# Performance work log

Measured on AMD Instinct MI355X. Metric: run time of the kernel, lower is better.

Reference implementation:

```python
import jax, jax.numpy as jnp
import numpy as np

SCALE = 0.2  # scale init arg, clipped to [0,1]


def _relative_corners(rank):
    # [2**rank, rank] matrix of +-1 corner coordinates
    return jnp.array([[float(int(c)) * 2.0 - 1.0 for c in format(i, '0%db' % rank)]
                      for i in range(2 ** rank)], dtype=jnp.float32)


def _affine_from_noise(random_u):
    # random_u: [B, 2**r, r] uniform(0,1) -> random_scale uniform(1-SCALE, 1)
    B, n, r = random_u.shape
    out_c = _relative_corners(r)                                  # [2^r, r]
    random_scale = (1.0 - SCALE) + SCALE * random_u
    src = out_c[None] * random_scale                              # [B, 2^r, r]
    ones_col = jnp.ones((B, n, 1), jnp.float32)
    A = jnp.broadcast_to(
        jnp.concatenate([out_c, jnp.ones((n, 1), jnp.float32)], -1)[None],
        (B, n, r + 1))                                            # output corners (homog.)
    Bmat = jnp.concatenate([src, ones_col], -1)                   # source corners (homog.)
    # least-squares solve A X = B  (matrix_solve_ls): X = (A^T A)^{-1} A^T B
    AtA = jnp.einsum('bni,bnj->bij', A, A)
    AtB = jnp.einsum('bni,bnj->bij', A, Bmat)
    X = jnp.linalg.solve(AtA, AtB)                                # [B, r+1, r+1]
    return jnp.transpose(X, (0, 2, 1))                            # transform, [B, r+1, r+1]


def _make_grid(transform, spatial_shape):
    # AffineGridWarper: output voxel coords normalized to [-1,1], affine-mapped,
    # then converted to source pixel coordinates [0, size-1].
    r = len(spatial_shape)
    axes = [jnp.linspace(-1.0, 1.0, s) for s in spatial_shape]
    mesh = jnp.stack(jnp.meshgrid(*axes, indexing='ij'), -1)      # [D,H,W,r]
    mesh_h = jnp.concatenate(
        [mesh, jnp.ones(tuple(spatial_shape) + (1,), jnp.float32)], -1)
    coords = jnp.einsum('dhwj,bij->bdhwi', mesh_h, transform[:, :r, :])  # [B,D,H,W,r]
    sizes = jnp.array(spatial_shape, jnp.float32)
    return (coords + 1.0) * (sizes - 1.0) * 0.5                   # pixel coords


def _resample_linear_zero(img, coords):
    # trilinear interpolation with zero boundary: out-of-range corners contribute 0
    # img: [B,D,H,W,C], coords: [B,D,H,W,3] (pixel coordinates)
    B = img.shape[0]
    sp = jnp.array(img.shape[1:4], jnp.int32)
    f = jnp.floor(coords)
    frac = coords - f                                             # [B,D,H,W,3]
    i0 = f.astype(jnp.int32)
    bidx = jnp.arange(B)[:, None, None, None]
    out = jnp.zeros(img.shape, img.dtype)
    for corner in range(8):  # fixed structural loop over 2^3 interpolation corners
        off = jnp.array([(corner >> 2) & 1, (corner >> 1) & 1, corner & 1], jnp.int32)
        idx = i0 + off
        valid = jnp.all((idx >= 0) & (idx < sp), axis=-1)         # [B,D,H,W]
        ci = jnp.clip(idx, 0, sp - 1)
        vals = img[bidx, ci[..., 0], ci[..., 1], ci[..., 2]]      # [B,D,H,W,C]
        w = jnp.prod(jnp.where(off == 1, frac, 1.0 - frac), axis=-1)
        w = w * valid.astype(img.dtype)
        out = out + vals * w[..., None]
    return out


def setup_inputs() -> dict:
    key = jax.random.key(0)
    k1, k2 = jax.random.split(key)
    input_tensor = jax.random.normal(k1, (8, 128, 128, 128, 1), dtype=jnp.float32)
    random_u = jax.random.uniform(k2, (8, 8, 3), dtype=jnp.float32)
    return {"input_tensor": input_tensor, "random_u": random_u}


def reference(input_tensor, random_u):
    transform = _affine_from_noise(random_u)                      # [B,4,4]
    grid = _make_grid(transform, input_tensor.shape[1:4])         # [B,D,H,W,3]
    return _resample_linear_zero(input_tensor, grid)
```

## Files before the change

### kernel.cpp

```cpp
#include <hip/hip_runtime.h>

#define NB   8
#define NS   128
#define VOX  (NS*NS*NS)

#define SD    13
#define SH    13
#define ROW_W 40
#define RST   (SH*ROW_W)
#define SLAB  (SD*RST)

typedef __attribute__((address_space(1))) const void gconst_t;
typedef __attribute__((address_space(3))) void lds_t;

__global__ __launch_bounds__(256) void warp_resample_kernel(
        const float* __restrict__ img, const float* __restrict__ u,
        float* __restrict__ out) {
    __shared__ __align__(16) float slab[SLAB];

    const int tid = threadIdx.x;
    const int bi   = blockIdx.x;
    const int b    =  bi & 7;
    const int idx  =  bi >> 3;
    const int wblk =  idx & 3;
    const int hblk = (idx >> 2) & 15;
    const int dblk =  idx >> 6;

    const float* ub = u + b * 24;
    float T[3][4];
#pragma unroll
    for (int i = 0; i < 3; ++i) {
        float v[8];
#pragma unroll
        for (int n = 0; n < 8; ++n) {
            const float sg = (n & (4 >> i)) ? 1.f : -1.f;
            v[n] = fmaf(sg * 0.025f, ub[n * 3 + i], sg * 0.1f);
        }
        const float a0 = v[0] + v[1], a1 = v[2] + v[3];
        const float a2 = v[4] + v[5], a3 = v[6] + v[7];
        const float d0 = v[1] - v[0], d1 = v[3] - v[2];
        const float d2 = v[5] - v[4], d3 = v[7] - v[6];
        const float A01 = a0 + a1, A23 = a2 + a3;
        T[i][0] = A23 - A01;
        T[i][1] = (a1 - a0) + (a3 - a2);
        T[i][2] = (d0 + d1) + (d2 + d3);
        T[i][3] = A01 + A23;
    }
    const float t00 = T[0][0], t01 = T[0][1], t02 = T[0][2], t03 = T[0][3];
    const float t10 = T[1][0], t11 = T[1][1], t12 = T[1][2], t13 = T[1][3];
    const float t20 = T[2][0], t21 = T[2][1], t22 = T[2][2], t23 = T[2][3];

    const int d0i = dblk << 3, h0i = hblk << 3, w0i = wblk << 5;
    const float inv = 2.0f / 127.0f;
    const float x0 = -1.f + d0i * inv, y0 = -1.f + h0i * inv, z0 = -1.f + w0i * inv;
    const float P0 = (t00 * x0 + t01 * y0 + t02 * z0 + t03 + 1.f) * 63.5f;
    const float P1 = (t10 * x0 + t11 * y0 + t12 * z0 + t13 + 1.f) * 63.5f;
    const float P2 = (t20 * x0 + t21 * y0 + t22 * z0 + t23 + 1.f) * 63.5f;

    const float mn0 = P0 + fminf(0.f,7.f*t00)+fminf(0.f,7.f*t01)+fminf(0.f,31.f*t02);
    const float mx0 = P0 + fmaxf(0.f,7.f*t00)+fmaxf(0.f,7.f*t01)+fmaxf(0.f,31.f*t02);
    const float mn1 = P1 + fminf(0.f,7.f*t10)+fminf(0.f,7.f*t11)+fminf(0.f,31.f*t12);
    const float mx1 = P1 + fmaxf(0.f,7.f*t10)+fmaxf(0.f,7.f*t11)+fmaxf(0.f,31.f*t12);
    const float mn2 = P2 + fminf(0.f,7.f*t20)+fminf(0.f,7.f*t21)+fminf(0.f,31.f*t22);
    const float mx2 = P2 + fmaxf(0.f,7.f*t20)+fmaxf(0.f,7.f*t21)+fmaxf(0.f,31.f*t22);

    const int i0mn = (int)floorf(mn0), i0mx = (int)floorf(mx0);
    const int i1mn = (int)floorf(mn1), i1mx = (int)floorf(mx1);
    const int i2mn = (int)floorf(mn2), i2mx = (int)floorf(mx2);

    const int d_lo = i0mn;
    const int h_lo = i1mn;
    const int ws   = (i2mn - 1) & ~3;
    const int Sd   = min(i0mx + 2 - d_lo, SD);
    const int Sh   = min(i1mx + 2 - h_lo, SH);

    const int allin = __builtin_amdgcn_readfirstlane(
        (d_lo >= 0 && d_lo + Sd <= NS &&
         h_lo >= 0 && h_lo + Sh <= NS &&
         ws   >= 0 && ws + ROW_W <= NS) ? 1 : 0);

    const float Pl0 = P0 - (float)d_lo;
    const float Pl1 = P1 - (float)h_lo;
    const float Pl2 = P2 - (float)ws;

    if (!allin) {
        float4* p = (float4*)slab;
        for (int i = tid; i < SLAB / 4; i += 256)
            p[i] = make_float4(0.f, 0.f, 0.f, 0.f);
        __syncthreads();
    }

    {
        const float* gb = img + (size_t)b * VOX;
        const int hi = tid / 10;
        const int c  = tid - hi * 10;
        const int wvbase = (tid & ~63) << 2;
        if (allin) {
            if (hi < Sh) {
                for (int di = 0; di < Sd; ++di) {
                    const float* g = gb + (((d_lo + di) * NS + (h_lo + hi)) * NS
                                           + ws + (c << 2));
                    __builtin_amdgcn_global_load_lds(
                        (gconst_t*)g, (lds_t*)(slab + di * RST + wvbase), 16, 0, 0);
                }
            }
        } else {
            const int  cc = ws + (c << 2);
            const bool ok = (hi < Sh) && ((unsigned)(h_lo + hi) < NS)
                                      && ((unsigned)cc <= NS - 4);
            if (ok) {
                for (int di = 0; di < Sd; ++di) {
                    if ((unsigned)(d_lo + di) < NS) {
                        const float* g = gb + (((d_lo + di) * NS + (h_lo + hi)) * NS
                                               + cc);
                        __builtin_amdgcn_global_load_lds(
                            (gconst_t*)g, (lds_t*)(slab + di * RST + wvbase), 16, 0, 0);
                    }
                }
            }
        }
    }
    __syncthreads();

    const int wl = tid & 31, hh = tid >> 5;
    float ql0 = Pl0 + hh * t01 + wl * t02;
    float ql1 = Pl1 + hh * t11 + wl * t12;
    float ql2 = Pl2 + hh * t21 + wl * t22;

    float res[8];
#pragma unroll
    for (int k = 0; k < 8; ++k) {
        const float f0 = floorf(ql0), f1 = floorf(ql1), f2 = floorf(ql2);
        const int   i0 = (int)f0,     i1 = (int)f1,     i2 = (int)f2;
        const float r0 = ql0 - f0,    r1 = ql1 - f1,    r2 = ql2 - f2;

        const int base = i0 * RST + i1 * ROW_W + i2;
        float a00 = slab[base],           b00 = slab[base + 1];
        float a01 = slab[base + ROW_W],   b01 = slab[base + ROW_W + 1];
        const int base2 = base + RST;
        float a10 = slab[base2],          b10 = slab[base2 + 1];
        float a11 = slab[base2 + ROW_W],  b11 = slab[base2 + ROW_W + 1];

        float e0 = fmaf(r2, b00 - a00, a00);
        float e1 = fmaf(r2, b01 - a01, a01);
        float e2 = fmaf(r2, b10 - a10, a10);
        float e3 = fmaf(r2, b11 - a11, a11);
        float c0 = fmaf(r1, e1 - e0, e0);
        float c1 = fmaf(r1, e3 - e2, e2);
        res[k] = fmaf(r0, c1 - c0, c0);

        ql0 += t00; ql1 += t10; ql2 += t20;
    }

    size_t ob = (((size_t)(b * NS + d0i) * NS + (h0i + hh)) * NS) + w0i + wl;
#pragma unroll
    for (int k = 0; k < 8; ++k)
        out[ob + (size_t)k * NS * NS] = res[k];
}

extern "C" void kernel_launch(void* const* d_in, const int* in_sizes, int n_in,
                              void* d_out, int out_size, void* d_ws, size_t ws_size,
                              hipStream_t stream) {
    const float* img = (const float*)d_in[0];
    const float* u   = (const float*)d_in[1];
    float* out = (float*)d_out;

    int blocks = NB * 16 * 16 * 4;
    warp_resample_kernel<<<blocks, 256, 0, stream>>>(img, u, out);
}
```

Baseline: 122.1 us.

## Halve depth tile per block and precompute affine transform in separate kernel

Each block now covers 4 depth slices instead of 8, which shrinks the LDS slab from 13 to 9 depth planes and doubles the grid size. The launch bounds now request 8 blocks per CU to raise occupancy. The per-batch affine transform is computed once by a tiny preceding kernel into a device global, replacing the per-block recomputation. The cost is an extra kernel launch and relatively more halo loading per output voxel.

```diff
diff --git a/kernel.cpp b/kernel.cpp
--- a/kernel.cpp
+++ b/kernel.cpp
@@ -4,7 +4,7 @@
 #define NS   128
 #define VOX  (NS*NS*NS)
 
-#define SD    13
+#define SD    9
 #define SH    13
 #define ROW_W 40
 #define RST   (SH*ROW_W)
@@ -13,56 +13,54 @@
 typedef __attribute__((address_space(1))) const void gconst_t;
 typedef __attribute__((address_space(3))) void lds_t;
 
-__global__ __launch_bounds__(256) void warp_resample_kernel(
-        const float* __restrict__ img, const float* __restrict__ u,
-        float* __restrict__ out) {
+__device__ float g_tw[96];
+
+__global__ void transform_kernel(const float* __restrict__ u) {
+    const int t = threadIdx.x;
+    if (t >= 96) return;
+    const int b = t / 12, e = t - b * 12;
+    const int i = e >> 2, j = e & 3;
+    float acc = 0.f;
+#pragma unroll
+    for (int n = 0; n < 8; ++n) {
+        const float ci = (n & (4 >> i)) ? 1.f : -1.f;
+        const float cj = (j < 3) ? ((n & (4 >> j)) ? 1.f : -1.f) : 1.f;
+        const float s  = 0.8f + 0.2f * u[(b * 8 + n) * 3 + i];
+        acc += cj * ci * s;
+    }
+    g_tw[b * 12 + e] = acc * 0.125f;
+}
+
+__global__ __launch_bounds__(256, 8) void warp_resample_kernel(
+        const float* __restrict__ img, float* __restrict__ out) {
     __shared__ __align__(16) float slab[SLAB];
 
     const int tid = threadIdx.x;
     const int bi   = blockIdx.x;
-    const int b    =  bi & 7;
+    const int b    = __builtin_amdgcn_readfirstlane(bi & 7);
     const int idx  =  bi >> 3;
     const int wblk =  idx & 3;
     const int hblk = (idx >> 2) & 15;
     const int dblk =  idx >> 6;
 
-    const float* ub = u + b * 24;
-    float T[3][4];
-#pragma unroll
-    for (int i = 0; i < 3; ++i) {
-        float v[8];
-#pragma unroll
-        for (int n = 0; n < 8; ++n) {
-            const float sg = (n & (4 >> i)) ? 1.f : -1.f;
-            v[n] = fmaf(sg * 0.025f, ub[n * 3 + i], sg * 0.1f);
-        }
-        const float a0 = v[0] + v[1], a1 = v[2] + v[3];
-        const float a2 = v[4] + v[5], a3 = v[6] + v[7];
-        const float d0 = v[1] - v[0], d1 = v[3] - v[2];
-        const float d2 = v[5] - v[4], d3 = v[7] - v[6];
-        const float A01 = a0 + a1, A23 = a2 + a3;
-        T[i][0] = A23 - A01;
-        T[i][1] = (a1 - a0) + (a3 - a2);
-        T[i][2] = (d0 + d1) + (d2 + d3);
-        T[i][3] = A01 + A23;
-    }
-    const float t00 = T[0][0], t01 = T[0][1], t02 = T[0][2], t03 = T[0][3];
-    const float t10 = T[1][0], t11 = T[1][1], t12 = T[1][2], t13 = T[1][3];
-    const float t20 = T[2][0], t21 = T[2][1], t22 = T[2][2], t23 = T[2][3];
+    const float* tw = g_tw + b * 12;
+    const float t00 = tw[0], t01 = tw[1], t02 = tw[2],  t03 = tw[3];
+    const float t10 = tw[4], t11 = tw[5], t12 = tw[6],  t13 = tw[7];
+    const float t20 = tw[8], t21 = tw[9], t22 = tw[10], t23 = tw[11];
 
-    const int d0i = dblk << 3, h0i = hblk << 3, w0i = wblk << 5;
+    const int d0i = dblk << 2, h0i = hblk << 3, w0i = wblk << 5;
     const float inv = 2.0f / 127.0f;
     const float x0 = -1.f + d0i * inv, y0 = -1.f + h0i * inv, z0 = -1.f + w0i * inv;
     const float P0 = (t00 * x0 + t01 * y0 + t02 * z0 + t03 + 1.f) * 63.5f;
     const float P1 = (t10 * x0 + t11 * y0 + t12 * z0 + t13 + 1.f) * 63.5f;
     const float P2 = (t20 * x0 + t21 * y0 + t22 * z0 + t23 + 1.f) * 63.5f;
 
-    const float mn0 = P0 + fminf(0.f,7.f*t00)+fminf(0.f,7.f*t01)+fminf(0.f,31.f*t02);
-    const float mx0 = P0 + fmaxf(0.f,7.f*t00)+fmaxf(0.f,7.f*t01)+fmaxf(0.f,31.f*t02);
-    const float mn1 = P1 + fminf(0.f,7.f*t10)+fminf(0.f,7.f*t11)+fminf(0.f,31.f*t12);
-    const float mx1 = P1 + fmaxf(0.f,7.f*t10)+fmaxf(0.f,7.f*t11)+fmaxf(0.f,31.f*t12);
-    const float mn2 = P2 + fminf(0.f,7.f*t20)+fminf(0.f,7.f*t21)+fminf(0.f,31.f*t22);
-    const float mx2 = P2 + fmaxf(0.f,7.f*t20)+fmaxf(0.f,7.f*t21)+fmaxf(0.f,31.f*t22);
+    const float mn0 = P0 + fminf(0.f,3.f*t00)+fminf(0.f,7.f*t01)+fminf(0.f,31.f*t02);
+    const float mx0 = P0 + fmaxf(0.f,3.f*t00)+fmaxf(0.f,7.f*t01)+fmaxf(0.f,31.f*t02);
+    const float mn1 = P1 + fminf(0.f,3.f*t10)+fminf(0.f,7.f*t11)+fminf(0.f,31.f*t12);
+    const float mx1 = P1 + fmaxf(0.f,3.f*t10)+fmaxf(0.f,7.f*t11)+fmaxf(0.f,31.f*t12);
+    const float mn2 = P2 + fminf(0.f,3.f*t20)+fminf(0.f,7.f*t21)+fminf(0.f,31.f*t22);
+    const float mx2 = P2 + fmaxf(0.f,3.f*t20)+fmaxf(0.f,7.f*t21)+fmaxf(0.f,31.f*t22);
 
     const int i0mn = (int)floorf(mn0), i0mx = (int)floorf(mx0);
     const int i1mn = (int)floorf(mn1), i1mx = (int)floorf(mx1);
@@ -127,9 +125,9 @@
     float ql1 = Pl1 + hh * t11 + wl * t12;
     float ql2 = Pl2 + hh * t21 + wl * t22;
 
-    float res[8];
+    float res[4];
 #pragma unroll
-    for (int k = 0; k < 8; ++k) {
+    for (int k = 0; k < 4; ++k) {
         const float f0 = floorf(ql0), f1 = floorf(ql1), f2 = floorf(ql2);
         const int   i0 = (int)f0,     i1 = (int)f1,     i2 = (int)f2;
         const float r0 = ql0 - f0,    r1 = ql1 - f1,    r2 = ql2 - f2;
@@ -154,7 +152,7 @@
 
     size_t ob = (((size_t)(b * NS + d0i) * NS + (h0i + hh)) * NS) + w0i + wl;
 #pragma unroll
-    for (int k = 0; k < 8; ++k)
+    for (int k = 0; k < 4; ++k)
         out[ob + (size_t)k * NS * NS] = res[k];
 }
 
@@ -165,6 +163,7 @@
     const float* u   = (const float*)d_in[1];
     float* out = (float*)d_out;
 
-    int blocks = NB * 16 * 16 * 4;
-    warp_resample_kernel<<<blocks, 256, 0, stream>>>(img, u, out);
+    transform_kernel<<<1, 128, 0, stream>>>(u);
+    int blocks = NB * 32 * 16 * 4;
+    warp_resample_kernel<<<blocks, 256, 0, stream>>>(img, out);
 }
```

Measured after the change: 125.3 us. 1.03x slower.

## Replace LDS slab staging with direct global gathers for trilinear resampling

Applied to the files above, without the earlier changes.

Removes the shared-memory slab, the global_load_lds staging and the block barrier, and gathers the eight corner samples for each output voxel directly from global memory. Interior blocks use an unguarded fast path. Border blocks use clamped indices with zero weights for out-of-range corners. This drops the zero-fill, the barrier and the extra LDS traffic, and allows more resident blocks. In exchange it relies on L1/L2 caching for neighbour reuse and issues many more scattered global loads per voxel.

```diff
diff --git a/kernel.cpp b/kernel.cpp
--- a/kernel.cpp
+++ b/kernel.cpp
@@ -4,20 +4,12 @@
 #define NS   128
 #define VOX  (NS*NS*NS)
 
-#define SD    13
-#define SH    13
-#define ROW_W 40
-#define RST   (SH*ROW_W)
-#define SLAB  (SD*RST)
 
-typedef __attribute__((address_space(1))) const void gconst_t;
-typedef __attribute__((address_space(3))) void lds_t;
+typedef float vf2 __attribute__((ext_vector_type(2)));
 
 __global__ __launch_bounds__(256) void warp_resample_kernel(
         const float* __restrict__ img, const float* __restrict__ u,
         float* __restrict__ out) {
-    __shared__ __align__(16) float slab[SLAB];
-
     const int tid = threadIdx.x;
     const int bi   = blockIdx.x;
     const int b    =  bi & 7;
@@ -68,88 +60,79 @@
     const int i1mn = (int)floorf(mn1), i1mx = (int)floorf(mx1);
     const int i2mn = (int)floorf(mn2), i2mx = (int)floorf(mx2);
 
-    const int d_lo = i0mn;
-    const int h_lo = i1mn;
-    const int ws   = (i2mn - 1) & ~3;
-    const int Sd   = min(i0mx + 2 - d_lo, SD);
-    const int Sh   = min(i1mx + 2 - h_lo, SH);
+    const int interior = __builtin_amdgcn_readfirstlane(
+        (i0mn >= 0 && i0mx <= NS - 2 &&
+         i1mn >= 0 && i1mx <= NS - 2 &&
+         i2mn >= 0 && i2mx <= NS - 2) ? 1 : 0);
 
-    const int allin = __builtin_amdgcn_readfirstlane(
-        (d_lo >= 0 && d_lo + Sd <= NS &&
-         h_lo >= 0 && h_lo + Sh <= NS &&
-         ws   >= 0 && ws + ROW_W <= NS) ? 1 : 0);
-
-    const float Pl0 = P0 - (float)d_lo;
-    const float Pl1 = P1 - (float)h_lo;
-    const float Pl2 = P2 - (float)ws;
-
-    if (!allin) {
-        float4* p = (float4*)slab;
-        for (int i = tid; i < SLAB / 4; i += 256)
-            p[i] = make_float4(0.f, 0.f, 0.f, 0.f);
-        __syncthreads();
-    }
-
-    {
-        const float* gb = img + (size_t)b * VOX;
-        const int hi = tid / 10;
-        const int c  = tid - hi * 10;
-        const int wvbase = (tid & ~63) << 2;
-        if (allin) {
-            if (hi < Sh) {
-                for (int di = 0; di < Sd; ++di) {
-                    const float* g = gb + (((d_lo + di) * NS + (h_lo + hi)) * NS
-                                           + ws + (c << 2));
-                    __builtin_amdgcn_global_load_lds(
-                        (gconst_t*)g, (lds_t*)(slab + di * RST + wvbase), 16, 0, 0);
-                }
-            }
-        } else {
-            const int  cc = ws + (c << 2);
-            const bool ok = (hi < Sh) && ((unsigned)(h_lo + hi) < NS)
-                                      && ((unsigned)cc <= NS - 4);
-            if (ok) {
-                for (int di = 0; di < Sd; ++di) {
-                    if ((unsigned)(d_lo + di) < NS) {
-                        const float* g = gb + (((d_lo + di) * NS + (h_lo + hi)) * NS
-                                               + cc);
-                        __builtin_amdgcn_global_load_lds(
-                            (gconst_t*)g, (lds_t*)(slab + di * RST + wvbase), 16, 0, 0);
-                    }
-                }
-            }
-        }
-    }
-    __syncthreads();
-
+    const float* gb = img + (size_t)b * VOX;
     const int wl = tid & 31, hh = tid >> 5;
-    float ql0 = Pl0 + hh * t01 + wl * t02;
-    float ql1 = Pl1 + hh * t11 + wl * t12;
-    float ql2 = Pl2 + hh * t21 + wl * t22;
+    float q0 = P0 + hh * t01 + wl * t02;
+    float q1 = P1 + hh * t11 + wl * t12;
+    float q2 = P2 + hh * t21 + wl * t22;
 
     float res[8];
+
+    if (interior) {
 #pragma unroll
-    for (int k = 0; k < 8; ++k) {
-        const float f0 = floorf(ql0), f1 = floorf(ql1), f2 = floorf(ql2);
-        const int   i0 = (int)f0,     i1 = (int)f1,     i2 = (int)f2;
-        const float r0 = ql0 - f0,    r1 = ql1 - f1,    r2 = ql2 - f2;
+        for (int k = 0; k < 8; ++k) {
+            const float f0 = floorf(q0), f1 = floorf(q1), f2 = floorf(q2);
+            const float r0 = q0 - f0,    r1 = q1 - f1,    r2 = q2 - f2;
+            const int vx = (int)fmaf(f0, 16384.f, fmaf(f1, 128.f, f2));
+            const float* p0 = gb + vx;
+            const float* p1 = gb + vx + NS * NS;
 
-        const int base = i0 * RST + i1 * ROW_W + i2;
-        float a00 = slab[base],           b00 = slab[base + 1];
-        float a01 = slab[base + ROW_W],   b01 = slab[base + ROW_W + 1];
-        const int base2 = base + RST;
-        float a10 = slab[base2],          b10 = slab[base2 + 1];
-        float a11 = slab[base2 + ROW_W],  b11 = slab[base2 + ROW_W + 1];
+            const float a00 = p0[0],       b00 = p0[1];
+            const float a01 = p0[NS],      b01 = p0[NS + 1];
+            const float a10 = p1[0],       b10 = p1[1];
+            const float a11 = p1[NS],      b11 = p1[NS + 1];
 
-        float e0 = fmaf(r2, b00 - a00, a00);
-        float e1 = fmaf(r2, b01 - a01, a01);
-        float e2 = fmaf(r2, b10 - a10, a10);
-        float e3 = fmaf(r2, b11 - a11, a11);
-        float c0 = fmaf(r1, e1 - e0, e0);
-        float c1 = fmaf(r1, e3 - e2, e2);
-        res[k] = fmaf(r0, c1 - c0, c0);
+            const float e0 = fmaf(r2, b00 - a00, a00);
+            const float e1 = fmaf(r2, b01 - a01, a01);
+            const float e2 = fmaf(r2, b10 - a10, a10);
+            const float e3 = fmaf(r2, b11 - a11, a11);
+            const float c0 = fmaf(r1, e1 - e0, e0);
+            const float c1 = fmaf(r1, e3 - e2, e2);
+            res[k] = fmaf(r0, c1 - c0, c0);
 
-        ql0 += t00; ql1 += t10; ql2 += t20;
+            q0 += t00; q1 += t10; q2 += t20;
+        }
+    } else {
+#pragma unroll
+        for (int k = 0; k < 8; ++k) {
+            const float f0 = floorf(q0), f1 = floorf(q1), f2 = floorf(q2);
+            const float r0 = q0 - f0,    r1 = q1 - f1,    r2 = q2 - f2;
+            const int   i0 = (int)f0,    i1 = (int)f1,    i2 = (int)f2;
+
+            const float wd0 = ((unsigned)i0       < NS) ? 1.f - r0 : 0.f;
+            const float wd1 = ((unsigned)(i0 + 1) < NS) ? r0       : 0.f;
+            const float wh0 = ((unsigned)i1       < NS) ? 1.f - r1 : 0.f;
+            const float wh1 = ((unsigned)(i1 + 1) < NS) ? r1       : 0.f;
+            const float ww0 = ((unsigned)i2       < NS) ? 1.f - r2 : 0.f;
+            const float ww1 = ((unsigned)(i2 + 1) < NS) ? r2       : 0.f;
+
+            const int da = min(max(i0,     0), NS - 1);
+            const int db = min(max(i0 + 1, 0), NS - 1);
+            const int ha = min(max(i1,     0), NS - 1);
+            const int hb = min(max(i1 + 1, 0), NS - 1);
+            const int wa = min(max(i2,     0), NS - 1);
+            const int wb = min(max(i2 + 1, 0), NS - 1);
+
+            const int ra00 = (da * NS + ha) * NS;
+            const int ra01 = (da * NS + hb) * NS;
+            const int ra10 = (db * NS + ha) * NS;
+            const int ra11 = (db * NS + hb) * NS;
+
+            const float e00 = gb[ra00 + wa] * ww0 + gb[ra00 + wb] * ww1;
+            const float e01 = gb[ra01 + wa] * ww0 + gb[ra01 + wb] * ww1;
+            const float e10 = gb[ra10 + wa] * ww0 + gb[ra10 + wb] * ww1;
+            const float e11 = gb[ra11 + wa] * ww0 + gb[ra11 + wb] * ww1;
+
+            res[k] = wd0 * fmaf(e00, wh0, e01 * wh1)
+                   + wd1 * fmaf(e10, wh0, e11 * wh1);
+
+            q0 += t00; q1 += t10; q2 += t20;
+        }
     }
 
     size_t ob = (((size_t)(b * NS + d0i) * NS + (h0i + hh)) * NS) + w0i + wl;
```

Measured after the change: 152.5 us. 1.25x slower.

## Give each wave a private LDS slab and overlap compute with staged loads

Applied to the files above, without the earlier changes.

Each block now has two waves, and each wave stages its own 13x7x40 slab through global_load_lds, so block-level barriers go away. Partial vmcnt waits let the interpolation of early depth slices start while later slices are still loading. Boundary blocks clamp the slab origin and mask out-of-range corner weights instead of zero-filling LDS. The grid has twice as many smaller blocks, and there is more redundant halo loading per output because each wave covers fewer rows.

```diff
diff --git a/kernel.cpp b/kernel.cpp
--- a/kernel.cpp
+++ b/kernel.cpp
@@ -4,27 +4,31 @@
 #define NS   128
 #define VOX  (NS*NS*NS)
 
-#define SD    13
-#define SH    13
-#define ROW_W 40
-#define RST   (SH*ROW_W)
-#define SLAB  (SD*RST)
+#define SD      13
+#define SHW     7
+#define ROW_W   40
+#define PLANE   (SHW*ROW_W)
+#define WSLICE  3640
+#define WSTRIDE 3840
+#define NLOAD   15
 
 typedef __attribute__((address_space(1))) const void gconst_t;
 typedef __attribute__((address_space(3))) void lds_t;
 
-__global__ __launch_bounds__(256) void warp_resample_kernel(
+__global__ __launch_bounds__(128) void warp_resample_kernel(
         const float* __restrict__ img, const float* __restrict__ u,
         float* __restrict__ out) {
-    __shared__ __align__(16) float slab[SLAB];
-
-    const int tid = threadIdx.x;
+    __shared__ __align__(16) float slab[2 * WSTRIDE];
+
+    const int tid  = threadIdx.x;
+    const int wid  = tid >> 6;
+    const int lane = tid & 63;
     const int bi   = blockIdx.x;
     const int b    =  bi & 7;
     const int idx  =  bi >> 3;
     const int wblk =  idx & 3;
-    const int hblk = (idx >> 2) & 15;
-    const int dblk =  idx >> 6;
+    const int hblk = (idx >> 2) & 31;
+    const int dblk =  idx >> 7;
 
     const float* ub = u + b * 24;
     float T[3][4];
@@ -50,109 +54,141 @@
     const float t10 = T[1][0], t11 = T[1][1], t12 = T[1][2], t13 = T[1][3];
     const float t20 = T[2][0], t21 = T[2][1], t22 = T[2][2], t23 = T[2][3];
 
-    const int d0i = dblk << 3, h0i = hblk << 3, w0i = wblk << 5;
+    const int d0i = dblk << 3, w0i = wblk << 5;
+    const int h0w = (hblk << 2) + (wid << 1);
     const float inv = 2.0f / 127.0f;
-    const float x0 = -1.f + d0i * inv, y0 = -1.f + h0i * inv, z0 = -1.f + w0i * inv;
+    const float x0 = -1.f + d0i * inv, y0 = -1.f + h0w * inv, z0 = -1.f + w0i * inv;
     const float P0 = (t00 * x0 + t01 * y0 + t02 * z0 + t03 + 1.f) * 63.5f;
     const float P1 = (t10 * x0 + t11 * y0 + t12 * z0 + t13 + 1.f) * 63.5f;
     const float P2 = (t20 * x0 + t21 * y0 + t22 * z0 + t23 + 1.f) * 63.5f;
 
-    const float mn0 = P0 + fminf(0.f,7.f*t00)+fminf(0.f,7.f*t01)+fminf(0.f,31.f*t02);
-    const float mx0 = P0 + fmaxf(0.f,7.f*t00)+fmaxf(0.f,7.f*t01)+fmaxf(0.f,31.f*t02);
-    const float mn1 = P1 + fminf(0.f,7.f*t10)+fminf(0.f,7.f*t11)+fminf(0.f,31.f*t12);
-    const float mx1 = P1 + fmaxf(0.f,7.f*t10)+fmaxf(0.f,7.f*t11)+fmaxf(0.f,31.f*t12);
-    const float mn2 = P2 + fminf(0.f,7.f*t20)+fminf(0.f,7.f*t21)+fminf(0.f,31.f*t22);
-    const float mx2 = P2 + fmaxf(0.f,7.f*t20)+fmaxf(0.f,7.f*t21)+fmaxf(0.f,31.f*t22);
-
-    const int i0mn = (int)floorf(mn0), i0mx = (int)floorf(mx0);
-    const int i1mn = (int)floorf(mn1), i1mx = (int)floorf(mx1);
-    const int i2mn = (int)floorf(mn2), i2mx = (int)floorf(mx2);
-
-    const int d_lo = i0mn;
-    const int h_lo = i1mn;
-    const int ws   = (i2mn - 1) & ~3;
-    const int Sd   = min(i0mx + 2 - d_lo, SD);
-    const int Sh   = min(i1mx + 2 - h_lo, SH);
-
+    const float mn0 = P0 + fminf(0.f,7.f*t00)+fminf(0.f,t01)+fminf(0.f,31.f*t02);
+    const float mn1 = P1 + fminf(0.f,7.f*t10)+fminf(0.f,t11)+fminf(0.f,31.f*t12);
+    const float mn2 = P2 + fminf(0.f,7.f*t20)+fminf(0.f,t21)+fminf(0.f,31.f*t22);
+    const int i0mn = (int)floorf(mn0);
+    const int i1mn = (int)floorf(mn1);
+    const int i2mn = (int)floorf(mn2);
+
+    const int wsu  = (i2mn - 1) & ~3;
+    const int d_lo = min(max(i0mn, 0), NS - SD);
+    const int h_lo = min(max(i1mn, 0), NS - SHW);
+    const int ws   = min(max(wsu, 0), NS - ROW_W);
     const int allin = __builtin_amdgcn_readfirstlane(
-        (d_lo >= 0 && d_lo + Sd <= NS &&
-         h_lo >= 0 && h_lo + Sh <= NS &&
-         ws   >= 0 && ws + ROW_W <= NS) ? 1 : 0);
+        (i0mn >= 0 && i0mn <= NS - SD && i1mn >= 0 && i1mn <= NS - SHW &&
+         wsu  >= 0 && wsu  <= NS - ROW_W) ? 1 : 0);
 
     const float Pl0 = P0 - (float)d_lo;
     const float Pl1 = P1 - (float)h_lo;
     const float Pl2 = P2 - (float)ws;
 
-    if (!allin) {
-        float4* p = (float4*)slab;
-        for (int i = tid; i < SLAB / 4; i += 256)
-            p[i] = make_float4(0.f, 0.f, 0.f, 0.f);
-        __syncthreads();
-    }
-
+    float* wslab = slab + wid * WSTRIDE;
     {
-        const float* gb = img + (size_t)b * VOX;
-        const int hi = tid / 10;
-        const int c  = tid - hi * 10;
-        const int wvbase = (tid & ~63) << 2;
-        if (allin) {
-            if (hi < Sh) {
-                for (int di = 0; di < Sd; ++di) {
-                    const float* g = gb + (((d_lo + di) * NS + (h_lo + hi)) * NS
-                                           + ws + (c << 2));
-                    __builtin_amdgcn_global_load_lds(
-                        (gconst_t*)g, (lds_t*)(slab + di * RST + wvbase), 16, 0, 0);
-                }
-            }
-        } else {
-            const int  cc = ws + (c << 2);
-            const bool ok = (hi < Sh) && ((unsigned)(h_lo + hi) < NS)
-                                      && ((unsigned)cc <= NS - 4);
-            if (ok) {
-                for (int di = 0; di < Sd; ++di) {
-                    if ((unsigned)(d_lo + di) < NS) {
-                        const float* g = gb + (((d_lo + di) * NS + (h_lo + hi)) * NS
-                                               + cc);
-                        __builtin_amdgcn_global_load_lds(
-                            (gconst_t*)g, (lds_t*)(slab + di * RST + wvbase), 16, 0, 0);
-                    }
-                }
-            }
+        const float* gwb = img + (size_t)b * VOX
+                         + (d_lo * NS + h_lo) * NS + ws;
+        int p = 0, rem = lane << 2;
+#pragma unroll
+        for (int j = 0; j < NLOAD; ++j) {
+            const int pp = min(p, SD - 1);
+            const int r  = (rem * 205) >> 13;
+            const float* g = gwb + pp * (NS * NS) + rem + r * 88;
+            __builtin_amdgcn_global_load_lds(
+                (gconst_t*)g, (lds_t*)(wslab + j * 256), 16, 0, 0);
+            rem += 256;
+            if (rem >= PLANE) { rem -= PLANE; ++p; }
         }
     }
-    __syncthreads();
-
-    const int wl = tid & 31, hh = tid >> 5;
-    float ql0 = Pl0 + hh * t01 + wl * t02;
-    float ql1 = Pl1 + hh * t11 + wl * t12;
-    float ql2 = Pl2 + hh * t21 + wl * t22;
+
+    const int wl = lane & 31, hw = lane >> 5;
+    float ql0 = Pl0 + hw * t01 + wl * t02;
+    float ql1 = Pl1 + hw * t11 + wl * t12;
+    float ql2 = Pl2 + hw * t21 + wl * t22;
 
     float res[8];
-#pragma unroll
-    for (int k = 0; k < 8; ++k) {
-        const float f0 = floorf(ql0), f1 = floorf(ql1), f2 = floorf(ql2);
-        const int   i0 = (int)f0,     i1 = (int)f1,     i2 = (int)f2;
-        const float r0 = ql0 - f0,    r1 = ql1 - f1,    r2 = ql2 - f2;
-
-        const int base = i0 * RST + i1 * ROW_W + i2;
-        float a00 = slab[base],           b00 = slab[base + 1];
-        float a01 = slab[base + ROW_W],   b01 = slab[base + ROW_W + 1];
-        const int base2 = base + RST;
-        float a10 = slab[base2],          b10 = slab[base2 + 1];
-        float a11 = slab[base2 + ROW_W],  b11 = slab[base2 + ROW_W + 1];
-
-        float e0 = fmaf(r2, b00 - a00, a00);
-        float e1 = fmaf(r2, b01 - a01, a01);
-        float e2 = fmaf(r2, b10 - a10, a10);
-        float e3 = fmaf(r2, b11 - a11, a11);
-        float c0 = fmaf(r1, e1 - e0, e0);
-        float c1 = fmaf(r1, e3 - e2, e2);
-        res[k] = fmaf(r0, c1 - c0, c0);
-
-        ql0 += t00; ql1 += t10; ql2 += t20;
-    }
-
-    size_t ob = (((size_t)(b * NS + d0i) * NS + (h0i + hh)) * NS) + w0i + wl;
+
+#define ITAP(k)                                                               \
+    {                                                                         \
+        const float f0 = floorf(ql0), f1 = floorf(ql1), f2 = floorf(ql2);     \
+        const float r0 = ql0 - f0, r1 = ql1 - f1, r2 = ql2 - f2;              \
+        const int base = (int)fmaf(f0, 280.f, fmaf(f1, 40.f, f2));            \
+        const float a00 = wslab[base],       b00 = wslab[base + 1];           \
+        const float a01 = wslab[base + 40],  b01 = wslab[base + 41];          \
+        const float a10 = wslab[base + 280], b10 = wslab[base + 281];         \
+        const float a11 = wslab[base + 320], b11 = wslab[base + 321];         \
+        const float e0 = fmaf(r2, b00 - a00, a00);                            \
+        const float e1 = fmaf(r2, b01 - a01, a01);                            \
+        const float e2 = fmaf(r2, b10 - a10, a10);                            \
+        const float e3 = fmaf(r2, b11 - a11, a11);                            \
+        const float c0 = fmaf(r1, e1 - e0, e0);                               \
+        const float c1 = fmaf(r1, e3 - e2, e2);                               \
+        res[k] = fmaf(r0, c1 - c0, c0);                                       \
+        ql0 += t00; ql1 += t10; ql2 += t20;                                   \
+    }
+
+    if (allin) {
+        asm volatile("s_waitcnt vmcnt(8)" ::: "memory"); ITAP(0)
+        asm volatile("s_waitcnt vmcnt(7)" ::: "memory"); ITAP(1)
+        asm volatile("s_waitcnt vmcnt(6)" ::: "memory"); ITAP(2)
+        asm volatile("s_waitcnt vmcnt(5)" ::: "memory"); ITAP(3)
+        asm volatile("s_waitcnt vmcnt(4)" ::: "memory"); ITAP(4)
+        asm volatile("s_waitcnt vmcnt(2)" ::: "memory"); ITAP(5)
+        asm volatile("s_waitcnt vmcnt(1)" ::: "memory"); ITAP(6)
+        asm volatile("s_waitcnt vmcnt(0)" ::: "memory"); ITAP(7)
+    } else {
+        asm volatile("s_waitcnt vmcnt(0)" ::: "memory");
+#pragma unroll
+        for (int k = 0; k < 8; ++k) {
+            const float f0 = floorf(ql0), f1 = floorf(ql1), f2 = floorf(ql2);
+            const float r0 = ql0 - f0, r1 = ql1 - f1, r2 = ql2 - f2;
+            const int i0 = (int)f0, i1 = (int)f1, i2 = (int)f2;
+
+            const float wd0 = ((unsigned)(i0 + d_lo)     < NS) ? 1.f - r0 : 0.f;
+            const float wd1 = ((unsigned)(i0 + d_lo + 1) < NS) ? r0       : 0.f;
+            const float wh0 = ((unsigned)(i1 + h_lo)     < NS) ? 1.f - r1 : 0.f;
+            const float wh1 = ((unsigned)(i1 + h_lo + 1) < NS) ? r1       : 0.f;
+            const float ww0 = ((unsigned)(i2 + ws)       < NS) ? 1.f - r2 : 0.f;
+            const float ww1 = ((unsigned)(i2 + ws + 1)   < NS) ? r2       : 0.f;
+
+            const int dI0 = min(max(i0,     0), SD  - 1);
+            const int dI1 = min(max(i0 + 1, 0), SD  - 1);
+            const int hI0 = min(max(i1,     0), SHW - 1);
+            const int hI1 = min(max(i1 + 1, 0), SHW - 1);
+            const int j0  = min(max(i2,     0), ROW_W - 1);
+            const int j1  = min(max(i2 + 1, 0), ROW_W - 1);
+            const bool same = (j1 == j0);
+
+            float acc = 0.f;
+            {
+                const int bb = dI0 * PLANE + hI0 * ROW_W + j0;
+                const float a = wslab[bb], bv = wslab[bb + 1];
+                const float rt = same ? a : bv;
+                acc = fmaf(fmaf(a, ww0, rt * ww1), wd0 * wh0, acc);
+            }
+            {
+                const int bb = dI0 * PLANE + hI1 * ROW_W + j0;
+                const float a = wslab[bb], bv = wslab[bb + 1];
+                const float rt = same ? a : bv;
+                acc = fmaf(fmaf(a, ww0, rt * ww1), wd0 * wh1, acc);
+            }
+            {
+                const int bb = dI1 * PLANE + hI0 * ROW_W + j0;
+                const float a = wslab[bb], bv = wslab[bb + 1];
+                const float rt = same ? a : bv;
+                acc = fmaf(fmaf(a, ww0, rt * ww1), wd1 * wh0, acc);
+            }
+            {
+                const int bb = dI1 * PLANE + hI1 * ROW_W + j0;
+                const float a = wslab[bb], bv = wslab[bb + 1];
+                const float rt = same ? a : bv;
+                acc = fmaf(fmaf(a, ww0, rt * ww1), wd1 * wh1, acc);
+            }
+            res[k] = acc;
+
+            ql0 += t00; ql1 += t10; ql2 += t20;
+        }
+    }
+#undef ITAP
+
+    size_t ob = (((size_t)(b * NS + d0i) * NS + (h0w + hw)) * NS) + w0i + wl;
 #pragma unroll
     for (int k = 0; k < 8; ++k)
         out[ob + (size_t)k * NS * NS] = res[k];
@@ -165,6 +201,6 @@
     const float* u   = (const float*)d_in[1];
     float* out = (float*)d_out;
 
-    int blocks = NB * 16 * 16 * 4;
-    warp_resample_kernel<<<blocks, 256, 0, stream>>>(img, u, out);
+    int blocks = NB * 16 * 32 * 4;
+    warp_resample_kernel<<<blocks, 128, 0, stream>>>(img, u, out);
 }
```

Result: slower. 150.5 us (+23.3%).
